# Kernel optimization log

Measured on AMD Instinct MI355X. Metric: run time of the kernel, lower is better.

The kernel has to match this reference:

```python
import jax, jax.numpy as jnp
import numpy as np

RANK = 8
LN_EPS = 1e-5


def setup_inputs() -> dict:
    key = jax.random.key(0)
    ks = jax.random.split(key, 8)
    B, T, D = 16, 1024, 1024
    A = 1024          # ada_dim
    I = 1024          # inter_dim
    OUT = D * RANK * 4  # 32768
    s = 0.02
    return {
        "x": jax.random.normal(ks[0], (B, T, D), jnp.float32),
        "ada_emb": jax.random.normal(ks[1], (B, A), jnp.float32),
        "base_up": jax.random.normal(ks[2], (D, D), jnp.float32) * s,
        "base_down": jax.random.normal(ks[3], (D, D), jnp.float32) * s,
        "ln_gamma": jnp.ones((A,), jnp.float32),
        "ln_beta": jnp.zeros((A,), jnp.float32),
        "W1": jax.random.normal(ks[4], (A, I), jnp.float32) / np.sqrt(A),
        "bias1": jnp.zeros((I,), jnp.float32),
        "W2": jax.random.normal(ks[5], (I, OUT), jnp.float32) / np.sqrt(I),
        "bias2": jnp.zeros((OUT,), jnp.float32),
    }


def reference(x, ada_emb, base_up, base_down, ln_gamma, ln_beta, W1, bias1, W2, bias2):
    B, T, D = x.shape
    R = RANK
    # norm_cond: LayerNorm over ada_dim (biased variance, eps=1e-5)
    mu = jnp.mean(ada_emb, axis=-1, keepdims=True)
    var = jnp.mean(jnp.square(ada_emb - mu), axis=-1, keepdims=True)
    c = (ada_emb - mu) / jnp.sqrt(var + LN_EPS) * ln_gamma + ln_beta
    # gen_weight: Linear -> GELU -> Linear
    h = jax.nn.gelu(c @ W1 + bias1, approximate=False)
    w = h @ W2 + bias2                         # (B, 4*D*R)
    a1, b1, a2, b2 = [t.reshape(B, D, R) for t in jnp.split(w, 4, axis=-1)]
    # down matvec: x @ (base_down + a2 @ b2^T), factored to avoid (B,D,D)
    u = jnp.einsum('btd,bdr->btr', x, a2)      # (B,T,R)
    mid = jnp.einsum('btd,dl->btl', x, base_down) + jnp.einsum('btr,blr->btl', u, b2)
    mid = jax.nn.gelu(mid, approximate=False)  # act_fn between layers
    # up matvec: (base_up + a1 @ b1^T) @ mid, factored
    v = jnp.einsum('blr,btl->btr', b1, mid)    # (B,T,R)
    out = jnp.einsum('btl,kl->btk', mid, base_up) + jnp.einsum('bkr,btr->btk', a1, v)
    return x + out  # residual
```

## Files before the change

kernel.cpp:

```cpp
#include <hip/hip_runtime.h>
#include <math.h>

#define DD 1024
#define NB 16
#define WSPLIT 16
#define HSPLIT 32

typedef unsigned short u16;
typedef __attribute__((ext_vector_type(8))) short short8;
typedef __attribute__((ext_vector_type(4))) float f32x4;

__device__ __forceinline__ float gelu_f(float x) {
  return 0.5f * x * (1.0f + erff(x * 0.70710678118654752440f));
}
__device__ __forceinline__ u16 f2bf(float f) {
  union { float f; unsigned u; } v; v.f = f;
  return (u16)((v.u + 0x7FFFu + ((v.u >> 16) & 1u)) >> 16);
}
__device__ __forceinline__ float bf2f(u16 b) {
  union { unsigned u; float f; } v; v.u = ((unsigned)b) << 16;
  return v.f;
}
__device__ __forceinline__ void gload_lds16(const u16* g, u16* l) {
  __builtin_amdgcn_global_load_lds(
      (const __attribute__((address_space(1))) void*)g,
      (__attribute__((address_space(3))) void*)l, 16, 0, 0);
}

#define VMCNT8   asm volatile("s_waitcnt vmcnt(8)" ::: "memory")
#define VMCNT0   asm volatile("s_waitcnt vmcnt(0)" ::: "memory")
#define BARRIER  asm volatile("s_barrier" ::: "memory")

__launch_bounds__(256)
__global__ void prep_kernel(const float* __restrict__ x, u16* __restrict__ xb,
                            const float* __restrict__ ada, const float* __restrict__ gamma,
                            const float* __restrict__ beta, float* __restrict__ c,
                            const float* __restrict__ bdn, u16* __restrict__ bdTb,
                            const float* __restrict__ bu, u16* __restrict__ bub) {
  __shared__ float smem[1056];
  int bid = blockIdx.x;
  int t = threadIdx.x;
  if (bid < 8192) {
    size_t i = (size_t)bid * 256 + t;
    const float4* xf = (const float4*)x;
    float4 v0 = xf[i * 2], v1 = xf[i * 2 + 1];
    short8 o;
    o[0] = (short)f2bf(v0.x); o[1] = (short)f2bf(v0.y);
    o[2] = (short)f2bf(v0.z); o[3] = (short)f2bf(v0.w);
    o[4] = (short)f2bf(v1.x); o[5] = (short)f2bf(v1.y);
    o[6] = (short)f2bf(v1.z); o[7] = (short)f2bf(v1.w);
    *(short8*)(xb + i * 8) = o;
  } else if (bid < 8208) {
    int b = bid - 8192;
    const float* row = ada + b * DD;
    float s = 0.f, s2 = 0.f;
    for (int i = t; i < DD; i += 256) { float v = row[i]; s += v; s2 += v * v; }
    for (int off = 32; off; off >>= 1) { s += __shfl_down(s, off); s2 += __shfl_down(s2, off); }
    float* rs = smem; float* rs2 = smem + 4;
    int wave = t >> 6, lane = t & 63;
    if (lane == 0) { rs[wave] = s; rs2[wave] = s2; }
    __syncthreads();
    if (t == 0) {
      float a = 0.f, a2 = 0.f;
      for (int w = 0; w < 4; w++) { a += rs[w]; a2 += rs2[w]; }
      rs[0] = a * (1.0f / DD); rs2[0] = a2 * (1.0f / DD);
    }
    __syncthreads();
    float mu = rs[0];
    float var = rs2[0] - mu * mu;
    float inv = rsqrtf(var + 1e-5f);
    for (int i = t; i < DD; i += 256)
      c[b * DD + i] = (row[i] - mu) * inv * gamma[i] + beta[i];
  } else if (bid < 9232) {
    int t2 = bid - 8208;
    int bx = (t2 & 31) * 32, by = (t2 >> 5) * 32;
    float (*tile)[33] = (float(*)[33])smem;
    int tx = t & 31, ty = t >> 5;
    for (int r = ty; r < 32; r += 8) tile[r][tx] = bdn[(size_t)(by + r) * DD + bx + tx];
    __syncthreads();
    for (int r = ty; r < 32; r += 8)
      bdTb[(size_t)(bx + r) * DD + by + tx] = f2bf(tile[tx][r]);
  } else {
    size_t i = (size_t)(bid - 9232) * 256 + t;
    const float4* bf = (const float4*)bu;
    float4 v0 = bf[i * 2], v1 = bf[i * 2 + 1];
    short8 o;
    o[0] = (short)f2bf(v0.x); o[1] = (short)f2bf(v0.y);
    o[2] = (short)f2bf(v0.z); o[3] = (short)f2bf(v0.w);
    o[4] = (short)f2bf(v1.x); o[5] = (short)f2bf(v1.y);
    o[6] = (short)f2bf(v1.z); o[7] = (short)f2bf(v1.w);
    *(short8*)(bub + i * 8) = o;
  }
}

__launch_bounds__(256)
__global__ void h_part_kernel(const float* __restrict__ c, const float* __restrict__ W1,
                              float* __restrict__ hpart) {
  int s = blockIdx.y;
  int j = blockIdx.x * 256 + threadIdx.x;
  int k0 = s * 32;
  __shared__ float cs[NB][32];
  for (int i = threadIdx.x; i < NB * 32; i += 256)
    cs[i >> 5][i & 31] = c[(size_t)(i >> 5) * DD + k0 + (i & 31)];
  __syncthreads();
  float acc[NB];
  #pragma unroll
  for (int b = 0; b < NB; b++) acc[b] = 0.f;
  #pragma unroll
  for (int al = 0; al < 32; al++) {
    float wv = W1[(size_t)(k0 + al) * DD + j];
    #pragma unroll
    for (int b = 0; b < NB; b++) acc[b] += cs[b][al] * wv;
  }
  #pragma unroll
  for (int b = 0; b < NB; b++)
    hpart[((size_t)s * NB + b) * DD + j] = acc[b];
}

__launch_bounds__(256)
__global__ void h_reduce_kernel(const float* __restrict__ hpart, const float* __restrict__ bias1,
                                float* __restrict__ h) {
  int idx = blockIdx.x * 256 + threadIdx.x;
  int j = idx & (DD - 1);
  float acc = bias1[j];
  #pragma unroll
  for (int s = 0; s < HSPLIT; s++) acc += hpart[(size_t)s * NB * DD + idx];
  h[idx] = gelu_f(acc);
}

__launch_bounds__(256)
__global__ void w_part_kernel(const float* __restrict__ h, const float* __restrict__ W2,
                              float* __restrict__ part) {
  int s = blockIdx.y;
  int j4 = blockIdx.x * 256 + threadIdx.x;
  int k0 = s * 64;
  int t = threadIdx.x;
  __shared__ float hl[NB][64];
  for (int i = t; i < NB * 64; i += 256) hl[i >> 6][i & 63] = h[(size_t)(i >> 6) * DD + k0 + (i & 63)];
  __syncthreads();
  float4 acc[NB];
  #pragma unroll
  for (int b = 0; b < NB; b++) acc[b] = float4{0.f, 0.f, 0.f, 0.f};
  const float4* W2v = (const float4*)W2;
  #pragma unroll 4
  for (int al = 0; al < 64; al++) {
    float4 wv = W2v[(size_t)(k0 + al) * 8192 + j4];
    #pragma unroll
    for (int b = 0; b < NB; b++) {
      float hb = hl[b][al];
      acc[b].x += hb * wv.x; acc[b].y += hb * wv.y;
      acc[b].z += hb * wv.z; acc[b].w += hb * wv.w;
    }
  }
  float4* pv = (float4*)part;
  #pragma unroll
  for (int b = 0; b < NB; b++)
    pv[((size_t)s * NB + b) * 8192 + j4] = acc[b];
}

__launch_bounds__(256)
__global__ void w_reduce_kernel(const float* __restrict__ part, const float* __restrict__ bias2,
                                float* __restrict__ w) {
  int idx = blockIdx.x * 256 + threadIdx.x;
  int j = idx & 32767;
  float acc = bias2[j];
  #pragma unroll
  for (int s = 0; s < WSPLIT; s++) acc += part[(size_t)s * NB * 32768 + idx];
  w[idx] = acc;
}

__launch_bounds__(256)
__global__ void pack_lora_kernel(const u16* __restrict__ src, const float* __restrict__ w,
                                 int aoff, int boff,
                                 u16* __restrict__ aext, u16* __restrict__ bext) {
  int b = blockIdx.y;
  const float* wb = w + (size_t)b * 32768;
  int t = threadIdx.x;
  short8 z = {};
  if (blockIdx.x < 16) {
    __shared__ float a2s[8192];
    for (int i = t; i < 8192; i += 256) a2s[i] = wb[aoff + i];
    __syncthreads();
    int row = blockIdx.x * 64 + (t >> 2);
    int q = t & 3;
    const u16* xr = src + ((size_t)b << 20) + (size_t)row * DD + q * 256;
    float acc[8] = {};
    #pragma unroll 4
    for (int kk = 0; kk < 32; kk++) {
      short8 xv = *(const short8*)(xr + kk * 8);
      #pragma unroll
      for (int e = 0; e < 8; e++) {
        float xf = bf2f((u16)xv[e]);
        int d = q * 256 + kk * 8 + e;
        #pragma unroll
        for (int r = 0; r < 8; r++) acc[r] += xf * a2s[d * 8 + r];
      }
    }
    #pragma unroll
    for (int r = 0; r < 8; r++) {
      acc[r] += __shfl_xor(acc[r], 1);
      acc[r] += __shfl_xor(acc[r], 2);
    }
    short8 ov = z;
    if (q == 0) {
      #pragma unroll
      for (int r = 0; r < 8; r++) ov[r] = (short)f2bf(acc[r]);
    }
    u16* orow = aext + ((size_t)b * 1024 + row) * 64 + q * 16;
    *(short8*)orow = ov;
    *(short8*)(orow + 8) = z;
  } else {
    for (int l = t; l < 1024; l += 256) {
      short8 ov;
      #pragma unroll
      for (int r = 0; r < 8; r++) ov[r] = (short)f2bf(wb[boff + l * 8 + r]);
      u16* orow = bext + ((size_t)b * 1024 + l) * 64;
      *(short8*)orow = ov;
      #pragma unroll
      for (int k = 1; k < 8; k++) *(short8*)(orow + k * 8) = z;
    }
  }
}

#define STAGE_A(KT, BUF) do { int kt_ = (KT);                                          \
    if (kt_ < 16) { int ks_ = kt_ * 64;                                                \
      _Pragma("unroll")                                                                \
      for (int c_ = 0; c_ < 4; c_++)                                                   \
        gload_lds16(Ab + (size_t)srow[c_] * DD + ks_ + se[c_], As[BUF] + ldsel[c_]);   \
    } else {                                                                           \
      _Pragma("unroll")                                                                \
      for (int c_ = 0; c_ < 4; c_++)                                                   \
        gload_lds16(Ae + (size_t)srow[c_] * 64 + se[c_], As[BUF] + ldsel[c_]);         \
    } } while (0)
#define STAGE_B(KT, BUF) do { int kt_ = (KT);                                          \
    if (kt_ < 16) { int ks_ = kt_ * 64;                                                \
      _Pragma("unroll")                                                                \
      for (int c_ = 0; c_ < 4; c_++)                                                   \
        gload_lds16(Bb + (size_t)srow[c_] * DD + ks_ + se[c_], Bs[BUF] + ldsel[c_]);   \
    } else {                                                                           \
      _Pragma("unroll")                                                                \
      for (int c_ = 0; c_ < 4; c_++)                                                   \
        gload_lds16(Be + (size_t)srow[c_] * 64 + se[c_], Bs[BUF] + ldsel[c_]);         \
    } } while (0)

template<int PHASE>
__launch_bounds__(512, 2)
__global__ void gemm256_kernel(const u16* __restrict__ A, const u16* __restrict__ BT,
                               const u16* __restrict__ Aext, const u16* __restrict__ Bext,
                               const u16* __restrict__ resid, void* __restrict__ Cout) {
  constexpr int BK = 64;
  constexpr int NT = 17;
  __shared__ __align__(16) u16 As[2][256 * BK];
  __shared__ __align__(16) u16 Bs[2][256 * BK];

  int orig = blockIdx.x;
  int logical = (orig & 7) * 32 + (orig >> 3);
  int b = logical >> 4;
  int tile = logical & 15;
  int tm = tile >> 2, tn = tile & 3;

  const u16* Ab = A + ((size_t)b << 20) + (size_t)(tm * 256) * DD;
  const u16* Bb = BT + (size_t)(tn * 256) * DD;
  const u16* Ae = Aext + ((size_t)b * 1024 + tm * 256) * 64;
  const u16* Be = Bext + ((size_t)b * 1024 + tn * 256) * 64;

  int t = threadIdx.x, lane = t & 63, g = lane >> 4, l15 = lane & 15;
  int wave = t >> 6;
  int wm = wave >> 2, wn = wave & 3;

  int srow[4], se[4], ldsel[4];
  #pragma unroll
  for (int c = 0; c < 4; c++) {
    int chunk = c * 512 + t;
    srow[c] = chunk >> 3;
    se[c] = ((chunk & 7) ^ (srow[c] & 7)) << 3;
    ldsel[c] = chunk * 8;
  }

  f32x4 acc[8][4] = {};

  STAGE_A(0, 0); STAGE_B(0, 0);
  STAGE_A(1, 1); STAGE_B(1, 1);
  VMCNT8;
  BARRIER;

  int cur = 0;
  #pragma unroll 1
  for (int kt = 0; kt < NT; kt++) {
    const u16* Ap = As[cur];
    const u16* Bp = Bs[cur];
    short8 afr[2][4], bf0[2][2], bf1[2][2];

    #pragma unroll
    for (int kk = 0; kk < 2; kk++) {
      #pragma unroll
      for (int i = 0; i < 4; i++) {
        int r = wm * 128 + i * 16 + l15;
        int e = (kk * 32 + g * 8) ^ ((r & 7) << 3);
        afr[kk][i] = *(const short8*)(Ap + r * BK + e);
      }
      #pragma unroll
      for (int j = 0; j < 2; j++) {
        int r = wn * 64 + j * 16 + l15;
        int e = (kk * 32 + g * 8) ^ ((r & 7) << 3);
        bf0[kk][j] = *(const short8*)(Bp + r * BK + e);
      }
    }
    BARRIER;
    __builtin_amdgcn_s_setprio(1);
    #pragma unroll
    for (int kk = 0; kk < 2; kk++)
      #pragma unroll
      for (int i = 0; i < 4; i++)
        #pragma unroll
        for (int j = 0; j < 2; j++)
          acc[i][j] = __builtin_amdgcn_mfma_f32_16x16x32_bf16(afr[kk][i], bf0[kk][j], acc[i][j], 0, 0, 0);
    __builtin_amdgcn_s_setprio(0);
    BARRIER;

    #pragma unroll
    for (int kk = 0; kk < 2; kk++)
      #pragma unroll
      for (int j = 0; j < 2; j++) {
        int r = wn * 64 + (j + 2) * 16 + l15;
        int e = (kk * 32 + g * 8) ^ ((r & 7) << 3);
        bf1[kk][j] = *(const short8*)(Bp + r * BK + e);
      }
    BARRIER;
    __builtin_amdgcn_s_setprio(1);
    #pragma unroll
    for (int kk = 0; kk < 2; kk++)
      #pragma unroll
      for (int i = 0; i < 4; i++)
        #pragma unroll
        for (int j = 0; j < 2; j++)
          acc[i][j + 2] = __builtin_amdgcn_mfma_f32_16x16x32_bf16(afr[kk][i], bf1[kk][j], acc[i][j + 2], 0, 0, 0);
    __builtin_amdgcn_s_setprio(0);
    BARRIER;

    if (kt + 2 < NT) STAGE_B(kt + 2, cur);
    #pragma unroll
    for (int kk = 0; kk < 2; kk++)
      #pragma unroll
      for (int i = 0; i < 4; i++) {
        int r = wm * 128 + (i + 4) * 16 + l15;
        int e = (kk * 32 + g * 8) ^ ((r & 7) << 3);
        afr[kk][i] = *(const short8*)(Ap + r * BK + e);
      }
    BARRIER;
    __builtin_amdgcn_s_setprio(1);
    #pragma unroll
    for (int kk = 0; kk < 2; kk++)
      #pragma unroll
      for (int i = 0; i < 4; i++)
        #pragma unroll
        for (int j = 0; j < 2; j++)
          acc[i + 4][j + 2] = __builtin_amdgcn_mfma_f32_16x16x32_bf16(afr[kk][i], bf1[kk][j], acc[i + 4][j + 2], 0, 0, 0);
    __builtin_amdgcn_s_setprio(0);
    BARRIER;

    if (kt + 2 < NT) STAGE_A(kt + 2, cur);
    __builtin_amdgcn_s_setprio(1);
    #pragma unroll
    for (int kk = 0; kk < 2; kk++)
      #pragma unroll
      for (int i = 0; i < 4; i++)
        #pragma unroll
        for (int j = 0; j < 2; j++)
          acc[i + 4][j] = __builtin_amdgcn_mfma_f32_16x16x32_bf16(afr[kk][i], bf0[kk][j], acc[i + 4][j], 0, 0, 0);
    __builtin_amdgcn_s_setprio(0);
    if (kt + 2 < NT) { VMCNT8; } else { VMCNT0; }
    BARRIER;

    cur ^= 1;
  }

  int r0 = tm * 256 + wm * 128;
  int c0 = tn * 256 + wn * 64;
  if (PHASE == 1) {
    u16* mid = (u16*)Cout + ((size_t)b << 20);
    #pragma unroll
    for (int i = 0; i < 8; i++)
      #pragma unroll
      for (int j = 0; j < 4; j++)
        #pragma unroll
        for (int r = 0; r < 4; r++) {
          int row = r0 + i * 16 + g * 4 + r;
          int col = c0 + j * 16 + l15;
          mid[(size_t)row * DD + col] = f2bf(gelu_f(acc[i][j][r]));
        }
  } else {
    float* out = (float*)Cout + ((size_t)b << 20);
    const u16* xb = resid + ((size_t)b << 20);
    #pragma unroll
    for (int i = 0; i < 8; i++)
      #pragma unroll
      for (int j = 0; j < 4; j++)
        #pragma unroll
        for (int r = 0; r < 4; r++) {
          int row = r0 + i * 16 + g * 4 + r;
          int col = c0 + j * 16 + l15;
          size_t idx = (size_t)row * DD + col;
          out[idx] = bf2f(xb[idx]) + acc[i][j][r];
        }
  }
}

extern "C" void kernel_launch(void* const* d_in, const int* in_sizes, int n_in,
                              void* d_out, int out_size, void* d_ws, size_t ws_size,
                              hipStream_t stream) {
  const float* x         = (const float*)d_in[0];
  const float* ada       = (const float*)d_in[1];
  const float* base_up   = (const float*)d_in[2];
  const float* base_down = (const float*)d_in[3];
  const float* gamma     = (const float*)d_in[4];
  const float* beta      = (const float*)d_in[5];
  const float* W1        = (const float*)d_in[6];
  const float* bias1     = (const float*)d_in[7];
  const float* W2        = (const float*)d_in[8];
  const float* bias2     = (const float*)d_in[9];
  float* out = (float*)d_out;
  char* ws = (char*)d_ws;

  float* c     = (float*)(ws);
  float* h     = (float*)(ws + 0x10000);
  float* w     = (float*)(ws + 0x20000);
  u16*   bdTb  = (u16*)  (ws + 0x220000);
  u16*   bub   = (u16*)  (ws + 0x420000);
  float* hpart = (float*)(ws + 0x620000);
  u16*   xb    = (u16*)  (ws + 0x820000);
  u16*   uext  = (u16*)  (ws + 0x2820000);
  u16*   b2ext = (u16*)  (ws + 0x2A20000);
  u16*   vext  = (u16*)  (ws + 0x2C20000);
  u16*   a1ext = (u16*)  (ws + 0x2E20000);
  u16*   mid   = (u16*)  (ws + 0x3020000);
  float* part  = (float*)(ws + 0x3020000);

  prep_kernel<<<dim3(9744), dim3(256), 0, stream>>>(x, xb, ada, gamma, beta, c,
                                                    base_down, bdTb, base_up, bub);
  h_part_kernel<<<dim3(4, HSPLIT), dim3(256), 0, stream>>>(c, W1, hpart);
  h_reduce_kernel<<<dim3(64), dim3(256), 0, stream>>>(hpart, bias1, h);
  w_part_kernel<<<dim3(32, WSPLIT), dim3(256), 0, stream>>>(h, W2, part);
  w_reduce_kernel<<<dim3(2048), dim3(256), 0, stream>>>(part, bias2, w);
  pack_lora_kernel<<<dim3(17, 16), dim3(256), 0, stream>>>(xb, w, 16384, 24576, uext, b2ext);
  gemm256_kernel<1><<<dim3(256), dim3(512), 0, stream>>>(xb, bdTb, uext, b2ext,
                                                         (const u16*)nullptr, (void*)mid);
  pack_lora_kernel<<<dim3(17, 16), dim3(256), 0, stream>>>(mid, w, 8192, 0, vext, a1ext);
  gemm256_kernel<2><<<dim3(256), dim3(512), 0, stream>>>(mid, bub, vext, a1ext, xb, (void*)out);
}
```

Before: 252.2 us.

## Switch GEMM to 32x32 MFMA, fuse h reduction into W2 stage, double split

The main GEMM kernels now use 32x32x16 bf16 MFMA tiles with f32x16 accumulators instead of 16x16x32 tiles. This means fewer LDS fragment loads per unit of MFMA work and a different epilogue layout. Separately, the h_reduce kernel is removed: each w_part block recomputes its slice of h (sum of partials, bias, GELU) directly from hpart. WSPLIT doubles to 32 for more parallelism in the W2 matvec, which doubles the partial-sum traffic that w_reduce must read, and the part buffer moves to avoid overlap.

```diff
diff --git a/kernel.cpp b/kernel.cpp
--- a/kernel.cpp
+++ b/kernel.cpp
@@ -3,12 +3,13 @@
 
 #define DD 1024
 #define NB 16
-#define WSPLIT 16
+#define WSPLIT 32
 #define HSPLIT 32
 
 typedef unsigned short u16;
 typedef __attribute__((ext_vector_type(8))) short short8;
 typedef __attribute__((ext_vector_type(4))) float f32x4;
+typedef __attribute__((ext_vector_type(16))) float f32x16;
 
 __device__ __forceinline__ float gelu_f(float x) {
   return 0.5f * x * (1.0f + erff(x * 0.70710678118654752440f));
@@ -118,41 +119,38 @@
 }
 
 __launch_bounds__(256)
-__global__ void h_reduce_kernel(const float* __restrict__ hpart, const float* __restrict__ bias1,
-                                float* __restrict__ h) {
-  int idx = blockIdx.x * 256 + threadIdx.x;
-  int j = idx & (DD - 1);
-  float acc = bias1[j];
-  #pragma unroll
-  for (int s = 0; s < HSPLIT; s++) acc += hpart[(size_t)s * NB * DD + idx];
-  h[idx] = gelu_f(acc);
-}
-
-__launch_bounds__(256)
-__global__ void w_part_kernel(const float* __restrict__ h, const float* __restrict__ W2,
-                              float* __restrict__ part) {
+__global__ void w_part_kernel(const float* __restrict__ hpart, const float* __restrict__ bias1,
+                              const float* __restrict__ W2, float* __restrict__ part) {
   int s = blockIdx.y;
   int j4 = blockIdx.x * 256 + threadIdx.x;
-  int k0 = s * 64;
+  int k0 = s * 32;
   int t = threadIdx.x;
-  __shared__ float hl[NB][64];
-  for (int i = t; i < NB * 64; i += 256) hl[i >> 6][i & 63] = h[(size_t)(i >> 6) * DD + k0 + (i & 63)];
+  __shared__ float hl[NB][32];
+  #pragma unroll
+  for (int v = 0; v < 2; v++) {
+    int i = t + v * 256;
+    int b = i >> 5, kk = i & 31;
+    float acc = bias1[k0 + kk];
+    #pragma unroll 8
+    for (int ss = 0; ss < HSPLIT; ss++) acc += hpart[((size_t)ss * NB + b) * DD + k0 + kk];
+    hl[b][kk] = gelu_f(acc);
+  }
   __syncthreads();
-  float4 acc[NB];
-  #pragma unroll
-  for (int b = 0; b < NB; b++) acc[b] = float4{0.f, 0.f, 0.f, 0.f};
+  f32x4 acc[NB];
+  #pragma unroll
+  for (int b = 0; b < NB; b++) acc[b] = f32x4{0.f, 0.f, 0.f, 0.f};
   const float4* W2v = (const float4*)W2;
-  #pragma unroll 4
-  for (int al = 0; al < 64; al++) {
+  #pragma unroll 8
+  for (int al = 0; al < 32; al++) {
     float4 wv = W2v[(size_t)(k0 + al) * 8192 + j4];
     #pragma unroll
     for (int b = 0; b < NB; b++) {
       float hb = hl[b][al];
-      acc[b].x += hb * wv.x; acc[b].y += hb * wv.y;
-      acc[b].z += hb * wv.z; acc[b].w += hb * wv.w;
-    }
-  }
-  float4* pv = (float4*)part;
+      acc[b][0] += hb * wv.x; acc[b][1] += hb * wv.y;
+      acc[b][2] += hb * wv.z; acc[b][3] += hb * wv.w;
+    }
+  }
+  f32x4* pv = (f32x4*)part;
   #pragma unroll
   for (int b = 0; b < NB; b++)
     pv[((size_t)s * NB + b) * 8192 + j4] = acc[b];
@@ -264,7 +262,8 @@
   const u16* Ae = Aext + ((size_t)b * 1024 + tm * 256) * 64;
   const u16* Be = Bext + ((size_t)b * 1024 + tn * 256) * 64;
 
-  int t = threadIdx.x, lane = t & 63, g = lane >> 4, l15 = lane & 15;
+  int t = threadIdx.x, lane = t & 63;
+  int l31 = lane & 31, kb = (lane >> 5) * 8;
   int wave = t >> 6;
   int wm = wave >> 2, wn = wave & 3;
 
@@ -277,7 +276,7 @@
     ldsel[c] = chunk * 8;
   }
 
-  f32x4 acc[8][4] = {};
+  f32x16 acc[4][2] = {};
 
   STAGE_A(0, 0); STAGE_B(0, 0);
   STAGE_A(1, 1); STAGE_B(1, 1);
@@ -289,85 +288,74 @@
   for (int kt = 0; kt < NT; kt++) {
     const u16* Ap = As[cur];
     const u16* Bp = Bs[cur];
-    short8 afr[2][4], bf0[2][2], bf1[2][2];
-
-    #pragma unroll
-    for (int kk = 0; kk < 2; kk++) {
-      #pragma unroll
-      for (int i = 0; i < 4; i++) {
-        int r = wm * 128 + i * 16 + l15;
-        int e = (kk * 32 + g * 8) ^ ((r & 7) << 3);
-        afr[kk][i] = *(const short8*)(Ap + r * BK + e);
+    short8 afr[2][4], bf0[4], bf1[4];
+
+    #pragma unroll
+    for (int ks = 0; ks < 4; ks++) {
+      #pragma unroll
+      for (int rt = 0; rt < 2; rt++) {
+        int r = wm * 128 + rt * 32 + l31;
+        int e = (ks * 16 + kb) ^ ((r & 7) << 3);
+        afr[rt][ks] = *(const short8*)(Ap + r * BK + e);
       }
-      #pragma unroll
-      for (int j = 0; j < 2; j++) {
-        int r = wn * 64 + j * 16 + l15;
-        int e = (kk * 32 + g * 8) ^ ((r & 7) << 3);
-        bf0[kk][j] = *(const short8*)(Bp + r * BK + e);
+      {
+        int r = wn * 64 + l31;
+        int e = (ks * 16 + kb) ^ ((r & 7) << 3);
+        bf0[ks] = *(const short8*)(Bp + r * BK + e);
       }
     }
     BARRIER;
     __builtin_amdgcn_s_setprio(1);
     #pragma unroll
-    for (int kk = 0; kk < 2; kk++)
-      #pragma unroll
-      for (int i = 0; i < 4; i++)
-        #pragma unroll
-        for (int j = 0; j < 2; j++)
-          acc[i][j] = __builtin_amdgcn_mfma_f32_16x16x32_bf16(afr[kk][i], bf0[kk][j], acc[i][j], 0, 0, 0);
+    for (int ks = 0; ks < 4; ks++)
+      #pragma unroll
+      for (int rt = 0; rt < 2; rt++)
+        acc[rt][0] = __builtin_amdgcn_mfma_f32_32x32x16_bf16(afr[rt][ks], bf0[ks], acc[rt][0], 0, 0, 0);
     __builtin_amdgcn_s_setprio(0);
     BARRIER;
 
     #pragma unroll
-    for (int kk = 0; kk < 2; kk++)
-      #pragma unroll
-      for (int j = 0; j < 2; j++) {
-        int r = wn * 64 + (j + 2) * 16 + l15;
-        int e = (kk * 32 + g * 8) ^ ((r & 7) << 3);
-        bf1[kk][j] = *(const short8*)(Bp + r * BK + e);
+    for (int ks = 0; ks < 4; ks++) {
+      int r = wn * 64 + 32 + l31;
+      int e = (ks * 16 + kb) ^ ((r & 7) << 3);
+      bf1[ks] = *(const short8*)(Bp + r * BK + e);
+    }
+    BARRIER;
+    __builtin_amdgcn_s_setprio(1);
+    #pragma unroll
+    for (int ks = 0; ks < 4; ks++)
+      #pragma unroll
+      for (int rt = 0; rt < 2; rt++)
+        acc[rt][1] = __builtin_amdgcn_mfma_f32_32x32x16_bf16(afr[rt][ks], bf1[ks], acc[rt][1], 0, 0, 0);
+    __builtin_amdgcn_s_setprio(0);
+    BARRIER;
+
+    if (kt + 2 < NT) STAGE_B(kt + 2, cur);
+    #pragma unroll
+    for (int ks = 0; ks < 4; ks++)
+      #pragma unroll
+      for (int rt = 0; rt < 2; rt++) {
+        int r = wm * 128 + (rt + 2) * 32 + l31;
+        int e = (ks * 16 + kb) ^ ((r & 7) << 3);
+        afr[rt][ks] = *(const short8*)(Ap + r * BK + e);
       }
     BARRIER;
     __builtin_amdgcn_s_setprio(1);
     #pragma unroll
-    for (int kk = 0; kk < 2; kk++)
-      #pragma unroll
-      for (int i = 0; i < 4; i++)
-        #pragma unroll
-        for (int j = 0; j < 2; j++)
-          acc[i][j + 2] = __builtin_amdgcn_mfma_f32_16x16x32_bf16(afr[kk][i], bf1[kk][j], acc[i][j + 2], 0, 0, 0);
-    __builtin_amdgcn_s_setprio(0);
-    BARRIER;
-
-    if (kt + 2 < NT) STAGE_B(kt + 2, cur);
-    #pragma unroll
-    for (int kk = 0; kk < 2; kk++)
-      #pragma unroll
-      for (int i = 0; i < 4; i++) {
-        int r = wm * 128 + (i + 4) * 16 + l15;
-        int e = (kk * 32 + g * 8) ^ ((r & 7) << 3);
-        afr[kk][i] = *(const short8*)(Ap + r * BK + e);
-      }
-    BARRIER;
-    __builtin_amdgcn_s_setprio(1);
-    #pragma unroll
-    for (int kk = 0; kk < 2; kk++)
-      #pragma unroll
-      for (int i = 0; i < 4; i++)
-        #pragma unroll
-        for (int j = 0; j < 2; j++)
-          acc[i + 4][j + 2] = __builtin_amdgcn_mfma_f32_16x16x32_bf16(afr[kk][i], bf1[kk][j], acc[i + 4][j + 2], 0, 0, 0);
+    for (int ks = 0; ks < 4; ks++)
+      #pragma unroll
+      for (int rt = 0; rt < 2; rt++)
+        acc[rt + 2][1] = __builtin_amdgcn_mfma_f32_32x32x16_bf16(afr[rt][ks], bf1[ks], acc[rt + 2][1], 0, 0, 0);
     __builtin_amdgcn_s_setprio(0);
     BARRIER;
 
     if (kt + 2 < NT) STAGE_A(kt + 2, cur);
     __builtin_amdgcn_s_setprio(1);
     #pragma unroll
-    for (int kk = 0; kk < 2; kk++)
-      #pragma unroll
-      for (int i = 0; i < 4; i++)
-        #pragma unroll
-        for (int j = 0; j < 2; j++)
-          acc[i + 4][j] = __builtin_amdgcn_mfma_f32_16x16x32_bf16(afr[kk][i], bf0[kk][j], acc[i + 4][j], 0, 0, 0);
+    for (int ks = 0; ks < 4; ks++)
+      #pragma unroll
+      for (int rt = 0; rt < 2; rt++)
+        acc[rt + 2][0] = __builtin_amdgcn_mfma_f32_32x32x16_bf16(afr[rt][ks], bf0[ks], acc[rt + 2][0], 0, 0, 0);
     __builtin_amdgcn_s_setprio(0);
     if (kt + 2 < NT) { VMCNT8; } else { VMCNT0; }
     BARRIER;
@@ -375,33 +363,33 @@
     cur ^= 1;
   }
 
-  int r0 = tm * 256 + wm * 128;
-  int c0 = tn * 256 + wn * 64;
+  int r0 = tm * 256 + wm * 128 + (lane >> 5) * 4;
+  int c0 = tn * 256 + wn * 64 + l31;
   if (PHASE == 1) {
     u16* mid = (u16*)Cout + ((size_t)b << 20);
     #pragma unroll
-    for (int i = 0; i < 8; i++)
-      #pragma unroll
-      for (int j = 0; j < 4; j++)
+    for (int rt = 0; rt < 4; rt++)
+      #pragma unroll
+      for (int ct = 0; ct < 2; ct++)
         #pragma unroll
-        for (int r = 0; r < 4; r++) {
-          int row = r0 + i * 16 + g * 4 + r;
-          int col = c0 + j * 16 + l15;
-          mid[(size_t)row * DD + col] = f2bf(gelu_f(acc[i][j][r]));
+        for (int reg = 0; reg < 16; reg++) {
+          int row = r0 + rt * 32 + (reg & 3) + 8 * (reg >> 2);
+          int col = c0 + ct * 32;
+          mid[(size_t)row * DD + col] = f2bf(gelu_f(acc[rt][ct][reg]));
         }
   } else {
     float* out = (float*)Cout + ((size_t)b << 20);
     const u16* xb = resid + ((size_t)b << 20);
     #pragma unroll
-    for (int i = 0; i < 8; i++)
-      #pragma unroll
-      for (int j = 0; j < 4; j++)
+    for (int rt = 0; rt < 4; rt++)
+      #pragma unroll
+      for (int ct = 0; ct < 2; ct++)
         #pragma unroll
-        for (int r = 0; r < 4; r++) {
-          int row = r0 + i * 16 + g * 4 + r;
-          int col = c0 + j * 16 + l15;
+        for (int reg = 0; reg < 16; reg++) {
+          int row = r0 + rt * 32 + (reg & 3) + 8 * (reg >> 2);
+          int col = c0 + ct * 32;
           size_t idx = (size_t)row * DD + col;
-          out[idx] = bf2f(xb[idx]) + acc[i][j][r];
+          out[idx] = bf2f(xb[idx]) + acc[rt][ct][reg];
         }
   }
 }
@@ -423,7 +411,6 @@
   char* ws = (char*)d_ws;
 
   float* c     = (float*)(ws);
-  float* h     = (float*)(ws + 0x10000);
   float* w     = (float*)(ws + 0x20000);
   u16*   bdTb  = (u16*)  (ws + 0x220000);
   u16*   bub   = (u16*)  (ws + 0x420000);
@@ -434,13 +421,12 @@
   u16*   vext  = (u16*)  (ws + 0x2C20000);
   u16*   a1ext = (u16*)  (ws + 0x2E20000);
   u16*   mid   = (u16*)  (ws + 0x3020000);
-  float* part  = (float*)(ws + 0x3020000);
+  float* part  = (float*)(ws + 0x5020000);
 
   prep_kernel<<<dim3(9744), dim3(256), 0, stream>>>(x, xb, ada, gamma, beta, c,
                                                     base_down, bdTb, base_up, bub);
   h_part_kernel<<<dim3(4, HSPLIT), dim3(256), 0, stream>>>(c, W1, hpart);
-  h_reduce_kernel<<<dim3(64), dim3(256), 0, stream>>>(hpart, bias1, h);
-  w_part_kernel<<<dim3(32, WSPLIT), dim3(256), 0, stream>>>(h, W2, part);
+  w_part_kernel<<<dim3(32, WSPLIT), dim3(256), 0, stream>>>(hpart, bias1, W2, part);
   w_reduce_kernel<<<dim3(2048), dim3(256), 0, stream>>>(part, bias2, w);
   pack_lora_kernel<<<dim3(17, 16), dim3(256), 0, stream>>>(xb, w, 16384, 24576, uext, b2ext);
   gemm256_kernel<1><<<dim3(256), dim3(512), 0, stream>>>(xb, bdTb, uext, b2ext,
```

Result: slower. 284.1 us (+12.7%).
